# Optimization experiments

Hardware: AMD Instinct MI355X
Metric: run time of the kernel (lower is better)

The kernel has to match this reference:

```python
import jax, jax.numpy as jnp
import numpy as np

# Static video grid (F, H, W); S = F*H*W tokens.
F_FRAMES, H_GRID, W_GRID = 9, 16, 28
DIM, N_HEADS = 1536, 12
HEAD_DIM = DIM // N_HEADS          # 128
ROT = HEAD_DIM // 2                # 64 complex pairs
EPS = 1e-6


def setup_inputs() -> dict:
    key = jax.random.key(0)
    ks = jax.random.split(key, 12)
    S = F_FRAMES * H_GRID * W_GRID
    scale = 0.02
    inp = {
        "x": jax.random.normal(ks[0], (1, S, DIM), jnp.float32),
        "seq_lens": jnp.array([S], jnp.int32),
        "grid_sizes": jnp.array([[F_FRAMES, H_GRID, W_GRID]], jnp.int32),
        "freqs": jax.random.normal(ks[1], (1024, ROT), jnp.float32),  # rope angles
        "Wq": jax.random.normal(ks[2], (DIM, DIM), jnp.float32) * scale,
        "bq": jnp.zeros((DIM,), jnp.float32),
        "Wk": jax.random.normal(ks[3], (DIM, DIM), jnp.float32) * scale,
        "bk": jnp.zeros((DIM,), jnp.float32),
        "Wv": jax.random.normal(ks[4], (DIM, DIM), jnp.float32) * scale,
        "bv": jnp.zeros((DIM,), jnp.float32),
        "Wo": jax.random.normal(ks[5], (DIM, DIM), jnp.float32) * scale,
        "bo": jnp.zeros((DIM,), jnp.float32),
        "gq": jnp.ones((DIM,), jnp.float32),
        "gk": jnp.ones((DIM,), jnp.float32),
    }
    return inp


def _rms_norm(h, g):
    # WanRMSNorm: h * rsqrt(mean(h^2) + eps) * weight
    var = jnp.mean(jnp.square(h), axis=-1, keepdims=True)
    return h * jax.lax.rsqrt(var + EPS) * g


def _rope_angles(freqs):
    # Split channel dim into temporal / height / width parts.
    c = ROT
    t_dim = c - 2 * (c // 3)  # 22
    s1 = c // 3               # 21
    temporal, height, width = freqs[:, :t_dim], freqs[:, t_dim:t_dim + s1], freqs[:, t_dim + s1:]
    t_ang = jnp.repeat(temporal[:F_FRAMES], H_GRID * W_GRID, axis=0)         # [S, 22]
    h_ang = jnp.tile(jnp.repeat(height[:H_GRID], W_GRID, axis=0), (F_FRAMES, 1))  # [S, 21]
    w_ang = jnp.tile(jnp.tile(width[:W_GRID], (H_GRID, 1)), (F_FRAMES, 1))        # [S, 21]
    return jnp.concatenate([t_ang, h_ang, w_ang], axis=-1)  # [S, c]


def _rope_apply(x, ang):
    # x: [B, S, n, d] viewed as complex pairs [B, S, n, d/2, 2]
    b, s, n, d = x.shape
    xp = x.reshape(b, s, n, d // 2, 2)
    xr, xi = xp[..., 0], xp[..., 1]
    cos = jnp.cos(ang)[None, :, None, :]
    sin = jnp.sin(ang)[None, :, None, :]
    out_r = xr * cos - xi * sin
    out_i = xr * sin + xi * cos
    return jnp.stack([out_r, out_i], axis=-1).reshape(b, s, n, d)


def reference(x, seq_lens, grid_sizes, freqs, Wq, bq, Wk, bk, Wv, bv, Wo, bo, gq, gk):
    b, s, _ = x.shape
    n, d = N_HEADS, HEAD_DIM
    q = _rms_norm(x @ Wq + bq, gq).reshape(b, s, n, d)
    k = _rms_norm(x @ Wk + bk, gk).reshape(b, s, n, d)
    v = (x @ Wv + bv).reshape(b, s, n, d)

    ang = _rope_angles(freqs)  # [S, d/2]
    rq = _rope_apply(q, ang)
    rk = _rope_apply(k, ang)

    # Causal frame-block mask: query in frame i attends to kv in frames <= i.
    frame_idx = jnp.arange(s) // (H_GRID * W_GRID)
    mask = frame_idx[None, :] <= frame_idx[:, None]  # [S_q, S_k]

    scale = 1.0 / jnp.sqrt(jnp.asarray(d, x.dtype))
    scores = jnp.einsum("bqnd,bknd->bnqk", rq, rk) * scale
    scores = jnp.where(mask[None, None], scores, jnp.asarray(-1e30, scores.dtype))
    probs = jax.nn.softmax(scores, axis=-1)
    attn = jnp.einsum("bnqk,bknd->bqnd", probs, v).reshape(b, s, n * d)
    return attn @ Wo + bo
```

## Files before the change

### kernel.cpp

```cpp
#include <hip/hip_runtime.h>
#include <stdint.h>

typedef unsigned short u16;
typedef unsigned int u32;
typedef __attribute__((ext_vector_type(8))) short bf16x8;
typedef __attribute__((ext_vector_type(4))) float f32x4;

#define S_LEN 4032
#define S_PAD 4096
#define DIMC  1536
#define HD    128
#define FRAME 448

static const size_t OFF_FLAG  = 0;
static const size_t OFF_CANON = 256;
static const size_t OFF_XB    = 524288;
static const size_t OFF_WT    = OFF_XB  + 12582912;
static const size_t OFF_WOT   = OFF_WT  + 14155776;
static const size_t OFF_YQ    = OFF_WOT + 4718592;
static const size_t OFF_YK    = OFF_YQ  + 12582912;
static const size_t OFF_VT    = OFF_YK  + 12582912;
static const size_t OFF_QH    = OFF_VT  + 12582912;
static const size_t OFF_KH    = OFF_QH  + 12386304;
static const size_t OFF_AT    = OFF_KH  + 12386304;
static const size_t WS_NEED   = OFF_AT  + 12582912;

#define C_BQ 0
#define C_BO 4608
#define C_GQ 6144
#define C_GK 7680
#define C_FR 9216
#define C_TOT 74752

__device__ __forceinline__ u16 f2bf(float f) {
  union { float f; u32 u; } v; v.f = f;
  u32 u = v.u;
  u32 r = (u + 0x7fffu + ((u >> 16) & 1u)) >> 16;
  return (u16)r;
}
__device__ __forceinline__ float bf2f(u16 h) {
  union { float f; u32 u; } v; v.u = ((u32)h) << 16;
  return v.f;
}

__device__ __forceinline__ void gld_lds16(const void* g, void* l) {
  __builtin_amdgcn_global_load_lds(
      (const __attribute__((address_space(1))) void*)(uintptr_t)g,
      (__attribute__((address_space(3))) void*)(u32)(uintptr_t)l,
      16, 0, 0);
}

__device__ __forceinline__ f32x4 mfma16(bf16x8 a, bf16x8 b, f32x4 c) {
  return __builtin_amdgcn_mfma_f32_16x16x32_bf16(a, b, c, 0, 0, 0);
}

__global__ void detect_dtype(const u16* __restrict__ x, int* __restrict__ flag) {
  __shared__ int cnt;
  if (threadIdx.x == 0) cnt = 0;
  __syncthreads();
  int e = (x[2 * threadIdx.x] >> 7) & 0xff;
  if (e > 150) atomicAdd(&cnt, 1);
  __syncthreads();
  if (threadIdx.x == 0) *flag = (cnt >= 8) ? 1 : 0;
}

__global__ void prep_small(const void* bq, const void* bk, const void* bv, const void* bo,
                           const void* gq, const void* gk, const void* fr,
                           float* __restrict__ canon, const int* __restrict__ flagp) {
  int fl = *flagp;
  for (int i = blockIdx.x * 256 + threadIdx.x; i < C_TOT; i += gridDim.x * 256) {
    const void* src; int j;
    if      (i < 1536) { src = bq; j = i; }
    else if (i < 3072) { src = bk; j = i - 1536; }
    else if (i < 4608) { src = bv; j = i - 3072; }
    else if (i < 6144) { src = bo; j = i - 4608; }
    else if (i < 7680) { src = gq; j = i - 6144; }
    else if (i < 9216) { src = gk; j = i - 7680; }
    else               { src = fr; j = i - 9216; }
    canon[i] = fl ? ((const float*)src)[j] : bf2f(((const u16*)src)[j]);
  }
}

__global__ void convert_x(const void* __restrict__ xin, u16* __restrict__ xb,
                          const int* __restrict__ flagp) {
  int fl = *flagp;
  int i = blockIdx.x * 256 + threadIdx.x;
  if (i >= (S_PAD * DIMC) / 8) return;
  size_t base = (size_t)i * 8;
  int row = (int)(base / DIMC);
  union { u16 h[8]; uint4 v; } u;
  if (row < S_LEN) {
    if (fl) {
      const float* xf = (const float*)xin + base;
      #pragma unroll
      for (int j = 0; j < 8; j++) u.h[j] = f2bf(xf[j]);
    } else {
      const u16* xh = (const u16*)xin + base;
      #pragma unroll
      for (int j = 0; j < 8; j++) u.h[j] = xh[j];
    }
  } else {
    #pragma unroll
    for (int j = 0; j < 8; j++) u.h[j] = 0;
  }
  ((uint4*)xb)[i] = u.v;
}

__global__ void transpose_w(const void* Wq, const void* Wk, const void* Wv, const void* Wo,
                            u16* __restrict__ wqkvt, u16* __restrict__ wot,
                            const int* __restrict__ flagp) {
  int fl = *flagp;
  int z = blockIdx.z;
  const void* W = (z == 0) ? Wq : (z == 1) ? Wk : (z == 2) ? Wv : Wo;
  u16* dst = (z < 3) ? (wqkvt + (size_t)z * DIMC * DIMC) : wot;
  __shared__ float tile[32][33];
  int tx = threadIdx.x, ty = threadIdx.y;
  int c = blockIdx.x * 32 + tx;
  #pragma unroll
  for (int i = 0; i < 4; i++) {
    int r = blockIdx.y * 32 + ty + i * 8;
    float v = fl ? ((const float*)W)[(size_t)r * DIMC + c]
                 : bf2f(((const u16*)W)[(size_t)r * DIMC + c]);
    tile[ty + i * 8][tx] = v;
  }
  __syncthreads();
  int k = blockIdx.y * 32 + tx;
  #pragma unroll
  for (int i = 0; i < 4; i++) {
    int n = blockIdx.x * 32 + ty + i * 8;
    dst[(size_t)n * DIMC + k] = f2bf(tile[tx][ty + i * 8]);
  }
}

template <int MODE>
__launch_bounds__(256, 2)
__global__ void gemm_bt(const u16* __restrict__ A, const u16* __restrict__ Bt,
                        const float* __restrict__ canon,
                        u16* __restrict__ Yq, u16* __restrict__ Yk, u16* __restrict__ Vt,
                        void* __restrict__ Out, const int* __restrict__ flagp) {
  const int bm0 = blockIdx.y * 128, bn0 = blockIdx.x * 128;
  const int tid = threadIdx.x, wave = tid >> 6, lane = tid & 63;
  const int wm = wave >> 1, wn = wave & 1;
  const int l15 = lane & 15, l4 = lane >> 4;
  __shared__ u16 sA[128 * 64];
  __shared__ u16 sB[128 * 64];
  f32x4 acc[4][4];
  #pragma unroll
  for (int i = 0; i < 4; i++)
    #pragma unroll
    for (int j = 0; j < 4; j++) acc[i][j] = (f32x4){0.f, 0.f, 0.f, 0.f};

  const u16* Ab = A  + (size_t)(bm0 + (lane >> 3)) * DIMC + (lane & 7) * 8;
  const u16* Bb = Bt + (size_t)(bn0 + (lane >> 3)) * DIMC + (lane & 7) * 8;

  for (int kt = 0; kt < DIMC; kt += 64) {
    __syncthreads();
    #pragma unroll
    for (int c = 0; c < 4; c++) {
      int g = wave * 4 + c;
      gld_lds16(Ab + (size_t)g * 8 * DIMC + kt, (char*)sA + g * 1024);
      gld_lds16(Bb + (size_t)g * 8 * DIMC + kt, (char*)sB + g * 1024);
    }
    __syncthreads();
    #pragma unroll
    for (int ks = 0; ks < 2; ks++) {
      const int ko = ks * 32 + l4 * 8;
      bf16x8 av[4], bvv[4];
      #pragma unroll
      for (int mt = 0; mt < 4; mt++) av[mt]  = *(const bf16x8*)(sA + (wm * 64 + mt * 16 + l15) * 64 + ko);
      #pragma unroll
      for (int nt = 0; nt < 4; nt++) bvv[nt] = *(const bf16x8*)(sB + (wn * 64 + nt * 16 + l15) * 64 + ko);
      #pragma unroll
      for (int mt = 0; mt < 4; mt++)
        #pragma unroll
        for (int nt = 0; nt < 4; nt++)
          acc[mt][nt] = mfma16(av[mt], bvv[nt], acc[mt][nt]);
    }
  }

  const int gm0 = bm0 + wm * 64;
  const int gn0 = bn0 + wn * 64;
  if (MODE == 0) {
    #pragma unroll
    for (int nt = 0; nt < 4; nt++) {
      int gn = gn0 + nt * 16 + l15;
      float b = canon[C_BQ + gn];
      #pragma unroll
      for (int mt = 0; mt < 4; mt++) {
        int gm = gm0 + mt * 16 + l4 * 4;
        if (gn < 1536) {
          #pragma unroll
          for (int r = 0; r < 4; r++)
            Yq[(size_t)(gm + r) * DIMC + gn] = f2bf(acc[mt][nt][r] + b);
        } else if (gn < 3072) {
          int g2 = gn - 1536;
          #pragma unroll
          for (int r = 0; r < 4; r++)
            Yk[(size_t)(gm + r) * DIMC + g2] = f2bf(acc[mt][nt][r] + b);
        } else {
          int g2 = gn - 3072;
          u32 lo = (u32)f2bf(acc[mt][nt][0] + b) | ((u32)f2bf(acc[mt][nt][1] + b) << 16);
          u32 hi = (u32)f2bf(acc[mt][nt][2] + b) | ((u32)f2bf(acc[mt][nt][3] + b) << 16);
          uint2 pk; pk.x = lo; pk.y = hi;
          *(uint2*)(Vt + (size_t)g2 * S_PAD + gm) = pk;
        }
      }
    }
  } else {
    const int fl = *flagp;
    #pragma unroll
    for (int nt = 0; nt < 4; nt++) {
      int gn = gn0 + nt * 16 + l15;
      float b = canon[C_BO + gn];
      #pragma unroll
      for (int mt = 0; mt < 4; mt++) {
        int gm = gm0 + mt * 16 + l4 * 4;
        #pragma unroll
        for (int r = 0; r < 4; r++) {
          int gr = gm + r;
          if (gr < S_LEN) {
            float v = acc[mt][nt][r] + b;
            if (fl) ((float*)Out)[(size_t)gr * DIMC + gn] = v;
            else    ((u16*)Out)[(size_t)gr * DIMC + gn] = f2bf(v);
          }
        }
      }
    }
  }
}

__global__ void norm_rope(const u16* __restrict__ Yq, const u16* __restrict__ Yk,
                          const float* __restrict__ canon, u16* __restrict__ Qh,
                          u16* __restrict__ Kh) {
  const int s = blockIdx.x;
  const int isq = (blockIdx.y == 0);
  const u16* Y = isq ? Yq : Yk;
  const float* g = canon + (isq ? C_GQ : C_GK);
  u16* Oh = isq ? Qh : Kh;
  const float sc = isq ? 0.08838834764831845f : 1.0f;
  const int tid = threadIdx.x, wave = tid >> 6, lane = tid & 63;
  __shared__ float row[DIMC];
  __shared__ float cs[64], sn[64];
  __shared__ float red[4];
  float ss = 0.f;
  for (int i = tid; i < DIMC; i += 256) {
    float v = bf2f(Y[(size_t)s * DIMC + i]);
    row[i] = v; ss += v * v;
  }
  #pragma unroll
  for (int d = 32; d; d >>= 1) ss += __shfl_down(ss, d, 64);
  if (lane == 0) red[wave] = ss;
  if (tid < 64) {
    int f_ = s / FRAME, hh = (s % FRAME) / 28, ww = s % 28;
    const float* fr = canon + C_FR;
    float a;
    if (tid < 22)      a = fr[f_ * 64 + tid];
    else if (tid < 43) a = fr[hh * 64 + tid];
    else               a = fr[ww * 64 + tid];
    float si, co;
    __sincosf(a, &si, &co);
    cs[tid] = co; sn[tid] = si;
  }
  __syncthreads();
  float rms = rsqrtf((red[0] + red[1] + red[2] + red[3]) * (1.f / 1536.f) + 1e-6f);
  for (int p = tid; p < 768; p += 256) {
    int head = p >> 6, jj = p & 63;
    float xr = row[2 * p]     * rms * g[2 * p];
    float xi = row[2 * p + 1] * rms * g[2 * p + 1];
    float c = cs[jj], s_ = sn[jj];
    u32 pk = (u32)f2bf((xr * c - xi * s_) * sc) | ((u32)f2bf((xr * s_ + xi * c) * sc) << 16);
    *(u32*)(Oh + ((size_t)head * S_LEN + s) * HD + 2 * jj) = pk;
  }
}

__launch_bounds__(256, 3)
__global__ void attn_v3(const u16* __restrict__ Qh, const u16* __restrict__ Kh,
                        const u16* __restrict__ Vt, u16* __restrict__ Ab) {
  const int tid = threadIdx.x, wave = tid >> 6, lane = tid & 63;
  const int l15 = lane & 15, l4 = lane >> 4;
  const int h = blockIdx.x % 12;
  const int qb = 62 - (blockIdx.x / 12);
  const int q0 = qb * 64;
  const int nkv = (q0 / FRAME + 1) * 7;
  __shared__ u16 sK[8192];
  __shared__ u16 sV[8192];
  __shared__ u16 sP[4][1024];
  u16* pw = sP[wave];

  int koff[4], voff[4];
  #pragma unroll
  for (int i = 0; i < 4; i++) {
    int s = (wave * 4 + i) * 64 + lane;
    int r = s >> 4, c = (s & 15) ^ (r & 15);
    koff[i] = r * HD + c * 8;
    int rv = s >> 3, cv = (s & 7) ^ (rv & 7);
    voff[i] = rv * S_PAD + cv * 8;
  }

  bf16x8 qf[4];
  {
    const u16* qp = Qh + ((size_t)h * S_LEN + q0 + wave * 16 + l15) * HD + l4 * 8;
    #pragma unroll
    for (int ks = 0; ks < 4; ks++) qf[ks] = *(const bf16x8*)(qp + ks * 32);
  }
  f32x4 o[8];
  #pragma unroll
  for (int i = 0; i < 8; i++) o[i] = (f32x4){0.f, 0.f, 0.f, 0.f};
  float m_i = -1e30f, l_i = 0.f;

  const u16* kb0 = Kh + (size_t)h * S_LEN * HD;
  const u16* vb0 = Vt + (size_t)h * HD * S_PAD;

  for (int t = 0; t < nkv; ++t) {
    __syncthreads();
    {
      const u16* kb = kb0 + (size_t)t * 64 * HD;
      const u16* vb = vb0 + t * 64;
      #pragma unroll
      for (int i = 0; i < 4; i++) {
        gld_lds16(kb + koff[i], (char*)sK + (wave * 4 + i) * 1024);
        gld_lds16(vb + voff[i], (char*)sV + (wave * 4 + i) * 1024);
      }
    }
    __syncthreads();

    f32x4 sT[4];
    #pragma unroll
    for (int nt = 0; nt < 4; nt++) sT[nt] = (f32x4){0.f, 0.f, 0.f, 0.f};
    #pragma unroll
    for (int ks = 0; ks < 4; ks++) {
      bf16x8 kf[4];
      #pragma unroll
      for (int nt = 0; nt < 4; nt++)
        kf[nt] = *(const bf16x8*)(sK + (nt * 16 + l15) * HD + (((ks * 4 + l4) ^ l15) * 8));
      #pragma unroll
      for (int nt = 0; nt < 4; nt++)
        sT[nt] = mfma16(kf[nt], qf[ks], sT[nt]);
    }

    float mloc = -1e30f;
    #pragma unroll
    for (int nt = 0; nt < 4; nt++)
      #pragma unroll
      for (int r = 0; r < 4; r++) mloc = fmaxf(mloc, sT[nt][r]);
    mloc = fmaxf(mloc, __shfl_xor(mloc, 16, 64));
    mloc = fmaxf(mloc, __shfl_xor(mloc, 32, 64));
    float mn = fmaxf(m_i, mloc);
    float alpha = __expf(m_i - mn);
    m_i = mn;
    float rs = 0.f;
    #pragma unroll
    for (int nt = 0; nt < 4; nt++)
      #pragma unroll
      for (int r = 0; r < 4; r++) {
        float p = __expf(sT[nt][r] - mn);
        sT[nt][r] = p; rs += p;
      }
    rs += __shfl_xor(rs, 16, 64);
    rs += __shfl_xor(rs, 32, 64);
    l_i = l_i * alpha + rs;
    #pragma unroll
    for (int i = 0; i < 8; i++)
      #pragma unroll
      for (int r = 0; r < 4; r++) o[i][r] *= alpha;

    #pragma unroll
    for (int nt = 0; nt < 4; nt++) {
      u32 lo = (u32)f2bf(sT[nt][0]) | ((u32)f2bf(sT[nt][1]) << 16);
      u32 hi = (u32)f2bf(sT[nt][2]) | ((u32)f2bf(sT[nt][3]) << 16);
      u32 off = (u32)((nt >> 1) * 512 + ((nt & 1) * 2 + (l4 >> 1)) * 128 + l15 * 8 + (l4 & 1) * 4);
      uint2 pk; pk.x = lo; pk.y = hi;
      *(uint2*)(pw + off) = pk;
    }
    #pragma unroll
    for (int ks2 = 0; ks2 < 2; ks2++) {
      bf16x8 pb = *(const bf16x8*)(pw + ks2 * 512 + lane * 8);
      #pragma unroll
      for (int vt = 0; vt < 8; vt++) {
        bf16x8 vf = *(const bf16x8*)(sV + (vt * 16 + l15) * 64 + (((ks2 * 4 + l4) ^ (l15 & 7)) * 8));
        o[vt] = mfma16(vf, pb, o[vt]);
      }
    }
  }

  float inv = 1.f / l_i;
  const size_t orow = (size_t)(q0 + wave * 16 + l15) * DIMC + (size_t)h * HD;
  #pragma unroll
  for (int vt = 0; vt < 8; vt++) {
    u32 lo = (u32)f2bf(o[vt][0] * inv) | ((u32)f2bf(o[vt][1] * inv) << 16);
    u32 hi = (u32)f2bf(o[vt][2] * inv) | ((u32)f2bf(o[vt][3] * inv) << 16);
    uint2 pk; pk.x = lo; pk.y = hi;
    *(uint2*)(Ab + orow + vt * 16 + l4 * 4) = pk;
  }
}

extern "C" void kernel_launch(void* const* d_in, const int* in_sizes, int n_in,
                              void* d_out, int out_size, void* d_ws, size_t ws_size,
                              hipStream_t stream) {
  if (ws_size < WS_NEED) return;
  char* ws = (char*)d_ws;
  int*   flag  = (int*)(ws + OFF_FLAG);
  float* canon = (float*)(ws + OFF_CANON);
  u16* xb    = (u16*)(ws + OFF_XB);
  u16* wqkvt = (u16*)(ws + OFF_WT);
  u16* wot   = (u16*)(ws + OFF_WOT);
  u16* yq    = (u16*)(ws + OFF_YQ);
  u16* yk    = (u16*)(ws + OFF_YK);
  u16* vt    = (u16*)(ws + OFF_VT);
  u16* qh    = (u16*)(ws + OFF_QH);
  u16* kh    = (u16*)(ws + OFF_KH);
  u16* ab    = (u16*)(ws + OFF_AT);

  const void* x  = d_in[0];
  const void* fr = d_in[3];
  const void* Wq = d_in[4];  const void* bq = d_in[5];
  const void* Wk = d_in[6];  const void* bk = d_in[7];
  const void* Wv = d_in[8];  const void* bv = d_in[9];
  const void* Wo = d_in[10]; const void* bo = d_in[11];
  const void* gq = d_in[12]; const void* gk = d_in[13];

  detect_dtype<<<1, 256, 0, stream>>>((const u16*)x, flag);
  prep_small<<<292, 256, 0, stream>>>(bq, bk, bv, bo, gq, gk, fr, canon, flag);
  convert_x<<<3072, 256, 0, stream>>>(x, xb, flag);
  transpose_w<<<dim3(48, 48, 4), dim3(32, 8), 0, stream>>>(Wq, Wk, Wv, Wo, wqkvt, wot, flag);
  gemm_bt<0><<<dim3(36, 32), 256, 0, stream>>>(xb, wqkvt, canon, yq, yk, vt, nullptr, flag);
  norm_rope<<<dim3(4032, 2), 256, 0, stream>>>(yq, yk, canon, qh, kh);
  attn_v3<<<756, 256, 0, stream>>>(qh, kh, vt, ab);
  gemm_bt<1><<<dim3(12, 32), 256, 0, stream>>>(ab, wot, canon, nullptr, nullptr, nullptr, d_out, flag);
}
```

Measured before the change: 386.0 us.

## Rework attention to two waves with two query tiles each; wave-per-row norm_rope

The attention kernel now runs 128-thread blocks where each wave handles two 16-row query tiles. Each K/V fragment read from shared memory is reused across two MFMAs, which halves LDS fragment traffic per FLOP, at the cost of more registers and fewer waves per block. The softmax switches to exp2f, with log2(e) folded into the Q scale. norm_rope is rewritten so each wave processes one token row in registers with shuffle reductions, removing shared memory and block barriers.

```diff
diff --git a/kernel.cpp b/kernel.cpp
--- a/kernel.cpp
+++ b/kernel.cpp
@@ -232,49 +232,51 @@
 __global__ void norm_rope(const u16* __restrict__ Yq, const u16* __restrict__ Yk,
                           const float* __restrict__ canon, u16* __restrict__ Qh,
                           u16* __restrict__ Kh) {
-  const int s = blockIdx.x;
+  const int tid = threadIdx.x, wave = tid >> 6, lane = tid & 63;
+  const int s = blockIdx.x * 4 + wave;
   const int isq = (blockIdx.y == 0);
   const u16* Y = isq ? Yq : Yk;
   const float* g = canon + (isq ? C_GQ : C_GK);
   u16* Oh = isq ? Qh : Kh;
-  const float sc = isq ? 0.08838834764831845f : 1.0f;
-  const int tid = threadIdx.x, wave = tid >> 6, lane = tid & 63;
-  __shared__ float row[DIMC];
-  __shared__ float cs[64], sn[64];
-  __shared__ float red[4];
+  const float sc = isq ? (0.08838834764831845f * 1.4426950408889634f) : 1.0f;
+
+  const u32* yrow = (const u32*)Y + (size_t)s * 768;
+  float xr[12], xi[12];
   float ss = 0.f;
-  for (int i = tid; i < DIMC; i += 256) {
-    float v = bf2f(Y[(size_t)s * DIMC + i]);
-    row[i] = v; ss += v * v;
-  }
-  #pragma unroll
-  for (int d = 32; d; d >>= 1) ss += __shfl_down(ss, d, 64);
-  if (lane == 0) red[wave] = ss;
-  if (tid < 64) {
-    int f_ = s / FRAME, hh = (s % FRAME) / 28, ww = s % 28;
-    const float* fr = canon + C_FR;
-    float a;
-    if (tid < 22)      a = fr[f_ * 64 + tid];
-    else if (tid < 43) a = fr[hh * 64 + tid];
-    else               a = fr[ww * 64 + tid];
-    float si, co;
-    __sincosf(a, &si, &co);
-    cs[tid] = co; sn[tid] = si;
-  }
-  __syncthreads();
-  float rms = rsqrtf((red[0] + red[1] + red[2] + red[3]) * (1.f / 1536.f) + 1e-6f);
-  for (int p = tid; p < 768; p += 256) {
-    int head = p >> 6, jj = p & 63;
-    float xr = row[2 * p]     * rms * g[2 * p];
-    float xi = row[2 * p + 1] * rms * g[2 * p + 1];
-    float c = cs[jj], s_ = sn[jj];
-    u32 pk = (u32)f2bf((xr * c - xi * s_) * sc) | ((u32)f2bf((xr * s_ + xi * c) * sc) << 16);
-    *(u32*)(Oh + ((size_t)head * S_LEN + s) * HD + 2 * jj) = pk;
-  }
-}
-
-__launch_bounds__(256, 3)
-__global__ void attn_v3(const u16* __restrict__ Qh, const u16* __restrict__ Kh,
+  #pragma unroll
+  for (int i = 0; i < 12; i++) {
+    u32 d = yrow[lane + 64 * i];
+    float a = bf2f((u16)(d & 0xffff));
+    float b = bf2f((u16)(d >> 16));
+    xr[i] = a; xi[i] = b;
+    ss += a * a + b * b;
+  }
+  #pragma unroll
+  for (int dd = 1; dd < 64; dd <<= 1) ss += __shfl_xor(ss, dd, 64);
+  float rms = rsqrtf(ss * (1.f / 1536.f) + 1e-6f);
+
+  int f_ = s / FRAME, hh = (s % FRAME) / 28, ww = s % 28;
+  const float* fr = canon + C_FR;
+  float a = (lane < 22) ? fr[f_ * 64 + lane]
+          : (lane < 43) ? fr[hh * 64 + lane]
+                        : fr[ww * 64 + lane];
+  float si, co;
+  __sincosf(a, &si, &co);
+
+  const float2* g2 = (const float2*)g;
+  #pragma unroll
+  for (int i = 0; i < 12; i++) {
+    int p = lane + 64 * i;
+    float2 gg = g2[p];
+    float r  = xr[i] * rms * gg.x;
+    float im = xi[i] * rms * gg.y;
+    u32 pk = (u32)f2bf((r * co - im * si) * sc) | ((u32)f2bf((r * si + im * co) * sc) << 16);
+    ((u32*)Oh)[((size_t)i * S_LEN + s) * 64 + lane] = pk;
+  }
+}
+
+__launch_bounds__(128, 2)
+__global__ void attn_v4(const u16* __restrict__ Qh, const u16* __restrict__ Kh,
                         const u16* __restrict__ Vt, u16* __restrict__ Ab) {
   const int tid = threadIdx.x, wave = tid >> 6, lane = tid & 63;
   const int l15 = lane & 15, l4 = lane >> 4;
@@ -285,28 +287,30 @@
   __shared__ u16 sK[8192];
   __shared__ u16 sV[8192];
   __shared__ u16 sP[4][1024];
-  u16* pw = sP[wave];
-
-  int koff[4], voff[4];
-  #pragma unroll
-  for (int i = 0; i < 4; i++) {
-    int s = (wave * 4 + i) * 64 + lane;
-    int r = s >> 4, c = (s & 15) ^ (r & 15);
-    koff[i] = r * HD + c * 8;
-    int rv = s >> 3, cv = (s & 7) ^ (rv & 7);
+
+  int koff[8], voff[8];
+  #pragma unroll
+  for (int i = 0; i < 8; i++) {
+    int c = i * 128 + tid;
+    int r = c >> 4, cc = (c & 15) ^ (r & 15);
+    koff[i] = r * HD + cc * 8;
+    int rv = c >> 3, cv = (c & 7) ^ (rv & 7);
     voff[i] = rv * S_PAD + cv * 8;
   }
 
-  bf16x8 qf[4];
-  {
-    const u16* qp = Qh + ((size_t)h * S_LEN + q0 + wave * 16 + l15) * HD + l4 * 8;
-    #pragma unroll
-    for (int ks = 0; ks < 4; ks++) qf[ks] = *(const bf16x8*)(qp + ks * 32);
-  }
-  f32x4 o[8];
-  #pragma unroll
-  for (int i = 0; i < 8; i++) o[i] = (f32x4){0.f, 0.f, 0.f, 0.f};
-  float m_i = -1e30f, l_i = 0.f;
+  bf16x8 qf[4][2];
+  #pragma unroll
+  for (int ct = 0; ct < 2; ct++) {
+    const u16* qp = Qh + ((size_t)h * S_LEN + q0 + wave * 32 + ct * 16 + l15) * HD + l4 * 8;
+    #pragma unroll
+    for (int ks = 0; ks < 4; ks++) qf[ks][ct] = *(const bf16x8*)(qp + ks * 32);
+  }
+  f32x4 o[8][2];
+  #pragma unroll
+  for (int i = 0; i < 8; i++)
+    #pragma unroll
+    for (int ct = 0; ct < 2; ct++) o[i][ct] = (f32x4){0.f, 0.f, 0.f, 0.f};
+  float m_i[2] = {-1e30f, -1e30f}, l_i[2] = {0.f, 0.f};
 
   const u16* kb0 = Kh + (size_t)h * S_LEN * HD;
   const u16* vb0 = Vt + (size_t)h * HD * S_PAD;
@@ -317,16 +321,18 @@
       const u16* kb = kb0 + (size_t)t * 64 * HD;
       const u16* vb = vb0 + t * 64;
       #pragma unroll
-      for (int i = 0; i < 4; i++) {
-        gld_lds16(kb + koff[i], (char*)sK + (wave * 4 + i) * 1024);
-        gld_lds16(vb + voff[i], (char*)sV + (wave * 4 + i) * 1024);
+      for (int i = 0; i < 8; i++) {
+        gld_lds16(kb + koff[i], (char*)sK + i * 2048 + wave * 1024);
+        gld_lds16(vb + voff[i], (char*)sV + i * 2048 + wave * 1024);
       }
     }
     __syncthreads();
 
-    f32x4 sT[4];
-    #pragma unroll
-    for (int nt = 0; nt < 4; nt++) sT[nt] = (f32x4){0.f, 0.f, 0.f, 0.f};
+    f32x4 sT[4][2];
+    #pragma unroll
+    for (int nt = 0; nt < 4; nt++)
+      #pragma unroll
+      for (int ct = 0; ct < 2; ct++) sT[nt][ct] = (f32x4){0.f, 0.f, 0.f, 0.f};
     #pragma unroll
     for (int ks = 0; ks < 4; ks++) {
       bf16x8 kf[4];
@@ -335,62 +341,80 @@
         kf[nt] = *(const bf16x8*)(sK + (nt * 16 + l15) * HD + (((ks * 4 + l4) ^ l15) * 8));
       #pragma unroll
       for (int nt = 0; nt < 4; nt++)
-        sT[nt] = mfma16(kf[nt], qf[ks], sT[nt]);
-    }
-
-    float mloc = -1e30f;
-    #pragma unroll
-    for (int nt = 0; nt < 4; nt++)
-      #pragma unroll
-      for (int r = 0; r < 4; r++) mloc = fmaxf(mloc, sT[nt][r]);
-    mloc = fmaxf(mloc, __shfl_xor(mloc, 16, 64));
-    mloc = fmaxf(mloc, __shfl_xor(mloc, 32, 64));
-    float mn = fmaxf(m_i, mloc);
-    float alpha = __expf(m_i - mn);
-    m_i = mn;
-    float rs = 0.f;
-    #pragma unroll
-    for (int nt = 0; nt < 4; nt++)
-      #pragma unroll
-      for (int r = 0; r < 4; r++) {
-        float p = __expf(sT[nt][r] - mn);
-        sT[nt][r] = p; rs += p;
+        #pragma unroll
+        for (int ct = 0; ct < 2; ct++)
+          sT[nt][ct] = mfma16(kf[nt], qf[ks][ct], sT[nt][ct]);
+    }
+
+    float alpha[2];
+    #pragma unroll
+    for (int ct = 0; ct < 2; ct++) {
+      float mloc = -1e30f;
+      #pragma unroll
+      for (int nt = 0; nt < 4; nt++)
+        #pragma unroll
+        for (int r = 0; r < 4; r++) mloc = fmaxf(mloc, sT[nt][ct][r]);
+      mloc = fmaxf(mloc, __shfl_xor(mloc, 16, 64));
+      mloc = fmaxf(mloc, __shfl_xor(mloc, 32, 64));
+      float mn = fmaxf(m_i[ct], mloc);
+      alpha[ct] = exp2f(m_i[ct] - mn);
+      m_i[ct] = mn;
+      float rs = 0.f;
+      #pragma unroll
+      for (int nt = 0; nt < 4; nt++)
+        #pragma unroll
+        for (int r = 0; r < 4; r++) {
+          float p = exp2f(sT[nt][ct][r] - mn);
+          sT[nt][ct][r] = p; rs += p;
+        }
+      rs += __shfl_xor(rs, 16, 64);
+      rs += __shfl_xor(rs, 32, 64);
+      l_i[ct] = l_i[ct] * alpha[ct] + rs;
+
+      u16* pw = sP[wave * 2 + ct];
+      #pragma unroll
+      for (int nt = 0; nt < 4; nt++) {
+        u32 lo = (u32)f2bf(sT[nt][ct][0]) | ((u32)f2bf(sT[nt][ct][1]) << 16);
+        u32 hi = (u32)f2bf(sT[nt][ct][2]) | ((u32)f2bf(sT[nt][ct][3]) << 16);
+        u32 off = (u32)((nt >> 1) * 512 + ((nt & 1) * 2 + (l4 >> 1)) * 128 + l15 * 8 + (l4 & 1) * 4);
+        uint2 pk; pk.x = lo; pk.y = hi;
+        *(uint2*)(pw + off) = pk;
       }
-    rs += __shfl_xor(rs, 16, 64);
-    rs += __shfl_xor(rs, 32, 64);
-    l_i = l_i * alpha + rs;
+    }
     #pragma unroll
     for (int i = 0; i < 8; i++)
       #pragma unroll
-      for (int r = 0; r < 4; r++) o[i][r] *= alpha;
-
-    #pragma unroll
-    for (int nt = 0; nt < 4; nt++) {
-      u32 lo = (u32)f2bf(sT[nt][0]) | ((u32)f2bf(sT[nt][1]) << 16);
-      u32 hi = (u32)f2bf(sT[nt][2]) | ((u32)f2bf(sT[nt][3]) << 16);
-      u32 off = (u32)((nt >> 1) * 512 + ((nt & 1) * 2 + (l4 >> 1)) * 128 + l15 * 8 + (l4 & 1) * 4);
-      uint2 pk; pk.x = lo; pk.y = hi;
-      *(uint2*)(pw + off) = pk;
-    }
+      for (int ct = 0; ct < 2; ct++)
+        #pragma unroll
+        for (int r = 0; r < 4; r++) o[i][ct][r] *= alpha[ct];
+
     #pragma unroll
     for (int ks2 = 0; ks2 < 2; ks2++) {
-      bf16x8 pb = *(const bf16x8*)(pw + ks2 * 512 + lane * 8);
+      bf16x8 pb[2];
+      #pragma unroll
+      for (int ct = 0; ct < 2; ct++)
+        pb[ct] = *(const bf16x8*)(sP[wave * 2 + ct] + ks2 * 512 + lane * 8);
       #pragma unroll
       for (int vt = 0; vt < 8; vt++) {
         bf16x8 vf = *(const bf16x8*)(sV + (vt * 16 + l15) * 64 + (((ks2 * 4 + l4) ^ (l15 & 7)) * 8));
-        o[vt] = mfma16(vf, pb, o[vt]);
+        #pragma unroll
+        for (int ct = 0; ct < 2; ct++)
+          o[vt][ct] = mfma16(vf, pb[ct], o[vt][ct]);
       }
     }
   }
 
-  float inv = 1.f / l_i;
-  const size_t orow = (size_t)(q0 + wave * 16 + l15) * DIMC + (size_t)h * HD;
-  #pragma unroll
-  for (int vt = 0; vt < 8; vt++) {
-    u32 lo = (u32)f2bf(o[vt][0] * inv) | ((u32)f2bf(o[vt][1] * inv) << 16);
-    u32 hi = (u32)f2bf(o[vt][2] * inv) | ((u32)f2bf(o[vt][3] * inv) << 16);
-    uint2 pk; pk.x = lo; pk.y = hi;
-    *(uint2*)(Ab + orow + vt * 16 + l4 * 4) = pk;
+  #pragma unroll
+  for (int ct = 0; ct < 2; ct++) {
+    float inv = 1.f / l_i[ct];
+    const size_t orow = (size_t)(q0 + wave * 32 + ct * 16 + l15) * DIMC + (size_t)h * HD;
+    #pragma unroll
+    for (int vt = 0; vt < 8; vt++) {
+      u32 lo = (u32)f2bf(o[vt][ct][0] * inv) | ((u32)f2bf(o[vt][ct][1] * inv) << 16);
+      u32 hi = (u32)f2bf(o[vt][ct][2] * inv) | ((u32)f2bf(o[vt][ct][3] * inv) << 16);
+      uint2 pk; pk.x = lo; pk.y = hi;
+      *(uint2*)(Ab + orow + vt * 16 + l4 * 4) = pk;
+    }
   }
 }
 
@@ -424,7 +448,7 @@
   convert_x<<<3072, 256, 0, stream>>>(x, xb, flag);
   transpose_w<<<dim3(48, 48, 4), dim3(32, 8), 0, stream>>>(Wq, Wk, Wv, Wo, wqkvt, wot, flag);
   gemm_bt<0><<<dim3(36, 32), 256, 0, stream>>>(xb, wqkvt, canon, yq, yk, vt, nullptr, flag);
-  norm_rope<<<dim3(4032, 2), 256, 0, stream>>>(yq, yk, canon, qh, kh);
-  attn_v3<<<756, 256, 0, stream>>>(qh, kh, vt, ab);
+  norm_rope<<<dim3(1008, 2), 256, 0, stream>>>(yq, yk, canon, qh, kh);
+  attn_v4<<<756, 128, 0, stream>>>(qh, kh, vt, ab);
   gemm_bt<1><<<dim3(12, 32), 256, 0, stream>>>(ab, wot, canon, nullptr, nullptr, nullptr, d_out, flag);
 }
```

Result: slower. 425.6 us (+10.3%).
